# Performance work log

Hardware: AMD Instinct MI355X
Metric: run time of the kernel (lower is better)

The kernel has to match this reference:

```python
import jax, jax.numpy as jnp
import numpy as np

# SpargeAttn / spas_sage2_attn_meansim block sizes
BLKQ, BLKK = 128, 64
NUM_HEADS = 8
SIMTHRESHD1 = 0.6
CDFTHRESHD = 0.98


def _block_meta(t, blk):
    # t: [B,H,S,D] -> block means [B,H,nb,D] and min-cosine-to-mean per block [B,H,nb]
    B, H, S, D = t.shape
    nb = S // blk
    tb = t.reshape(B, H, nb, blk, D)
    m = tb.mean(axis=3)
    tn = tb / (jnp.linalg.norm(tb, axis=-1, keepdims=True) + 1e-6)
    mn = m / (jnp.linalg.norm(m, axis=-1, keepdims=True) + 1e-6)
    cos = jnp.einsum('bhnkd,bhnd->bhnk', tn, mn)
    return m, cos.min(axis=-1)


def _meansim_sparse_attention(q, k, v, scale):
    # Block-sparse attention with mean-similarity pruning (SpargeAttn meansim).
    qm, qsim = _block_meta(q, BLKQ)          # [B,H,nq,D], [B,H,nq]
    km, ksim = _block_meta(k, BLKK)          # [B,H,nk,D], [B,H,nk]
    q_self = qsim > SIMTHRESHD1              # self-similar Q blocks -> mean is representative
    k_self = ksim > SIMTHRESHD1
    # pooled attention map over block means
    pooled = jax.nn.softmax(jnp.einsum('bhqd,bhkd->bhqk', qm, km) * scale, axis=-1)
    # per Q-block row: keep highest-prob K blocks until cumulative mass >= cdfthreshd
    order = jnp.argsort(-pooled, axis=-1)
    sp = jnp.take_along_axis(pooled, order, axis=-1)
    csum = jnp.cumsum(sp, axis=-1)
    keep_sorted = (csum - sp) < CDFTHRESHD   # always keeps at least the top block
    inv = jnp.argsort(order, axis=-1)
    keep = jnp.take_along_axis(keep_sorted, inv, axis=-1)  # [B,H,nq,nk]
    # conservative fallback: non-self-similar Q/K blocks are never pruned
    block_mask = keep | (~q_self)[..., None] | (~k_self)[:, :, None, :]
    tok_mask = jnp.repeat(jnp.repeat(block_mask, BLKQ, axis=2), BLKK, axis=3)
    s = jnp.einsum('bhqd,bhkd->bhqk', q, k) * scale
    s = jnp.where(tok_mask, s, -jnp.inf)
    p = jax.nn.softmax(s, axis=-1)
    return jnp.einsum('bhqk,bhkd->bhqd', p, v)


def setup_inputs() -> dict:
    key = jax.random.key(0)
    B, L, C = 2, 2048, 512
    ks = jax.random.split(key, 3)
    x = jax.random.normal(ks[0], (B, L, C), jnp.float32)
    Wqkv = jax.random.normal(ks[1], (C, 3 * C), jnp.float32) * (C ** -0.5)
    bqkv = jnp.zeros((3 * C,), jnp.float32)
    Wproj = jax.random.normal(ks[2], (C, C), jnp.float32) * (C ** -0.5)
    bproj = jnp.zeros((C,), jnp.float32)
    return {"x": x, "Wqkv": Wqkv, "bqkv": bqkv, "Wproj": Wproj, "bproj": bproj}


def reference(x, Wqkv, bqkv, Wproj, bproj):
    B, L, C = x.shape
    H = NUM_HEADS
    D = C // H
    scale = D ** -0.5
    qkv = (x @ Wqkv + bqkv).reshape(B, L, 3, H, D)
    qkv = jnp.transpose(qkv, (2, 0, 3, 1, 4))  # [3,B,H,L,D]
    q, k, v = qkv[0], qkv[1], qkv[2]
    o = _meansim_sparse_attention(q, k, v, scale)  # [B,H,L,D]
    o = jnp.transpose(o, (0, 2, 1, 3)).reshape(B, L, C)
    return o @ Wproj + bproj
```

## Files before the change

kernel.cpp:

```cpp
#include <hip/hip_runtime.h>
#include <math.h>

typedef unsigned short ushortT;
typedef unsigned int uintT;
typedef __attribute__((ext_vector_type(8))) short short8;
typedef __attribute__((ext_vector_type(16))) float f32x16;
#define MFMA32(a, b, c) __builtin_amdgcn_mfma_f32_32x32x16_bf16((a), (b), (c), 0, 0, 0)


#define LOG2E 1.4426950408889634f

static __device__ __forceinline__ ushortT f2b(float f) {
    union { float f; uintT u; } v; v.f = f;
    uintT u = v.u;
    u += 0x7fffu + ((u >> 16) & 1u);
    return (ushortT)(u >> 16);
}
static __device__ __forceinline__ uintT pack2(float a, float b) {
    return (uintT)f2b(a) | ((uintT)f2b(b) << 16);
}
static __device__ __forceinline__ uintT pack2t(float a, float b) {
    union { float f; uintT u; } x0, x1; x0.f = a; x1.f = b;
    return __builtin_amdgcn_perm(x1.u, x0.u, 0x07060302u);
}
static __device__ __forceinline__ float blo(uintT u) {
    union { uintT u; float f; } v; v.u = u << 16; return v.f;
}
static __device__ __forceinline__ float bhi(uintT u) {
    union { uintT u; float f; } v; v.u = u & 0xffff0000u; return v.f;
}
static __device__ __forceinline__ f32x16 zero16() {
    f32x16 z;
    #pragma unroll
    for (int i = 0; i < 16; ++i) z[i] = 0.f;
    return z;
}

#define B_N 2
#define H_N 8
#define L_N 2048
#define NQB 16
#define NKB 32

__global__ __launch_bounds__(256) void prep_kernel(
    const float* __restrict__ x, ushortT* __restrict__ xb,
    const float* __restrict__ Wq, ushortT* __restrict__ Wqt,
    const float* __restrict__ Wp, ushortT* __restrict__ Wpt) {
    const int bid = blockIdx.x, t = threadIdx.x;
    __shared__ float tile[32][33];
    if (bid < 2048) {
        int i = (bid * 256 + t) * 4;
        float4 v = *(const float4*)(x + i);
        uint2 o; o.x = pack2(v.x, v.y); o.y = pack2(v.z, v.w);
        *(uint2*)(xb + i) = o;
        return;
    }
    const float* W; ushortT* Wt; int C, c0, r0;
    if (bid < 2816) {
        const int b = bid - 2048;
        W = Wq; Wt = Wqt; C = 1536;
        c0 = (b % 48) * 32; r0 = (b / 48) * 32;
    } else {
        const int b = bid - 2816;
        W = Wp; Wt = Wpt; C = 512;
        c0 = (b & 15) * 32; r0 = (b >> 4) * 32;
    }
    const int tx = t & 31, ty = t >> 5;
    #pragma unroll
    for (int i = 0; i < 4; ++i)
        tile[ty + 8 * i][tx] = W[(size_t)(r0 + ty + 8 * i) * C + c0 + tx];
    __syncthreads();
    #pragma unroll
    for (int i = 0; i < 4; ++i) {
        int rr = ty + 8 * i;
        Wt[(size_t)(c0 + rr) * 512 + r0 + tx] = f2b(tile[tx][rr]);
    }
}

__global__ __launch_bounds__(256) void qkv_gemm_kernel(
    const ushortT* __restrict__ xb, const ushortT* __restrict__ wt,
    const float* __restrict__ bias,
    ushortT* __restrict__ qb, ushortT* __restrict__ kbuf, ushortT* __restrict__ vt,
    float* __restrict__ qm, float* __restrict__ km) {
    __shared__ __align__(16) ushortT As[2][128 * 40];
    __shared__ __align__(16) ushortT Bs[2][64 * 40];
    __shared__ float sumbuf[4][64];
    const int t = threadIdx.x;
    const int l = t & 63, w = t >> 6;
    const int lm = l & 31, lh = l >> 5;
    const int rowbase = blockIdx.y * 128;
    const int colbase = blockIdx.x * 64;

    f32x16 acc[2];
    acc[0] = zero16(); acc[1] = zero16();

    const int r = t >> 1, half = t & 1;
    const ushortT* Ag = xb + (size_t)(rowbase + r) * 512 + half * 16;
    const int soA = r * 40 + half * 16;
    const int rb = t >> 2, q4 = t & 3;
    const ushortT* Bg = wt + (size_t)(colbase + rb) * 512 + q4 * 8;
    const int soB = rb * 40 + q4 * 8;

    uint4 a0, a1, b0;
    a0 = *(const uint4*)(Ag); a1 = *(const uint4*)(Ag + 8);
    b0 = *(const uint4*)(Bg);
    *(uint4*)(&As[0][soA]) = a0; *(uint4*)(&As[0][soA] + 8) = a1;
    *(uint4*)(&Bs[0][soB]) = b0;

    for (int k0 = 0; k0 < 512; k0 += 32) {
        const int cur = (k0 >> 5) & 1;
        __syncthreads();
        if (k0 < 480) {
            a0 = *(const uint4*)(Ag + k0 + 32); a1 = *(const uint4*)(Ag + k0 + 40);
            b0 = *(const uint4*)(Bg + k0 + 32);
        }
        #pragma unroll
        for (int ks = 0; ks < 2; ++ks) {
            const int ko = 16 * ks + 8 * lh;
            short8 af  = *(const short8*)(&As[cur][(32 * w + lm) * 40 + ko]);
            short8 b_0 = *(const short8*)(&Bs[cur][lm * 40 + ko]);
            short8 b_1 = *(const short8*)(&Bs[cur][(32 + lm) * 40 + ko]);
            acc[0] = MFMA32(af, b_0, acc[0]);
            acc[1] = MFMA32(af, b_1, acc[1]);
        }
        if (k0 < 480) {
            const int nxt = cur ^ 1;
            *(uint4*)(&As[nxt][soA]) = a0; *(uint4*)(&As[nxt][soA] + 8) = a1;
            *(uint4*)(&Bs[nxt][soB]) = b0;
        }
    }

    const int which = blockIdx.x >> 3;
    const int h = blockIdx.x & 7;
    const int by = blockIdx.y;
    const int b = by >> 4;
    const size_t hb = (size_t)(b * 8 + h);
    float bias2[2];
    #pragma unroll
    for (int nt = 0; nt < 2; ++nt) bias2[nt] = bias[colbase + 32 * nt + lm];
    float msum[2] = {0.f, 0.f};
    #pragma unroll
    for (int nt = 0; nt < 2; ++nt) {
        const int dd = 32 * nt + lm;
        #pragma unroll
        for (int rg = 0; rg < 16; ++rg) {
            const int row_local = 32 * w + (rg & 3) + 8 * (rg >> 2) + 4 * lh;
            const int ll = (rowbase + row_local) & 2047;
            float val = acc[nt][rg] + bias2[nt];
            if (which == 0) {
                val *= 0.125f;
                msum[nt] += val;
                qb[(hb * 2048 + ll) * 64 + dd] = f2b(val * LOG2E);
            } else if (which == 1) {
                msum[nt] += val;
                kbuf[(hb * 2048 + ll) * 64 + dd] = f2b(val);
            } else {
                vt[hb * 131072 + (size_t)(ll >> 6) * 4096 + dd * 64 + (ll & 63)] = f2b(val);
            }
        }
    }
    if (which == 2) return;
    #pragma unroll
    for (int nt = 0; nt < 2; ++nt) {
        float s = msum[nt] + __shfl_xor(msum[nt], 32);
        if (l < 32) sumbuf[w][32 * nt + lm] = s;
    }
    __syncthreads();
    if (which == 0) {
        if (t < 64) {
            const int qbi = by & 15;
            qm[(hb * 16 + qbi) * 64 + t] =
                (sumbuf[0][t] + sumbuf[1][t] + sumbuf[2][t] + sumbuf[3][t]) * (1.0f / 128.0f);
        }
    } else {
        if (t < 128) {
            const int d = t & 63, pair = t >> 6;
            const int kbi = 2 * (by & 15) + pair;
            km[(hb * 32 + kbi) * 64 + d] =
                (sumbuf[2 * pair][d] + sumbuf[2 * pair + 1][d]) * (1.0f / 64.0f);
        }
    }
}

__global__ __launch_bounds__(256) void cos_kernel(const ushortT* __restrict__ qb,
                                                  const ushortT* __restrict__ kbuf,
                                                  const float* __restrict__ qm,
                                                  const float* __restrict__ km,
                                                  float* __restrict__ qs,
                                                  float* __restrict__ ks) {
    const int bh = blockIdx.y, t = threadIdx.x;
    const int l = t & 63, w = t >> 6;
    __shared__ float mS[64];
    __shared__ float wmin[4];
    if (blockIdx.z == 0) {
        if (blockIdx.x >= 16) return;
        const int qbk = blockIdx.x;
        if (t < 64) mS[t] = qm[((size_t)bh * 16 + qbk) * 64 + t];
        __syncthreads();
        float qn = 0.f;
        #pragma unroll
        for (int d = 0; d < 64; ++d) qn += mS[d] * mS[d];
        qn = sqrtf(qn);
        const int tok = t >> 1, half = t & 1;
        const ushortT* qrow = qb + ((size_t)bh * 2048 + qbk * 128 + tok) * 64 + half * 32;
        float dot = 0.f, nn = 0.f;
        #pragma unroll
        for (int c = 0; c < 4; ++c) {
            uint4 u = *(const uint4*)(qrow + c * 8);
            const int db = half * 32 + c * 8;
            float f0 = blo(u.x), f1 = bhi(u.x), f2 = blo(u.y), f3 = bhi(u.y);
            float f4 = blo(u.z), f5 = bhi(u.z), f6 = blo(u.w), f7 = bhi(u.w);
            dot += f0 * mS[db] + f1 * mS[db + 1] + f2 * mS[db + 2] + f3 * mS[db + 3]
                 + f4 * mS[db + 4] + f5 * mS[db + 5] + f6 * mS[db + 6] + f7 * mS[db + 7];
            nn += f0 * f0 + f1 * f1 + f2 * f2 + f3 * f3 + f4 * f4 + f5 * f5 + f6 * f6 + f7 * f7;
        }
        dot += __shfl_xor(dot, 1);
        nn += __shfl_xor(nn, 1);
        float cosv = dot / ((sqrtf(nn) + 1e-6f) * (qn + 1e-6f));
        #pragma unroll
        for (int off = 1; off < 64; off <<= 1) cosv = fminf(cosv, __shfl_xor(cosv, off));
        if (l == 0) wmin[w] = cosv;
        __syncthreads();
        if (t == 0)
            qs[bh * 16 + qbk] = fminf(fminf(wmin[0], wmin[1]), fminf(wmin[2], wmin[3]));
    } else {
        const int kbk = blockIdx.x;
        if (t < 64) mS[t] = km[((size_t)bh * 32 + kbk) * 64 + t];
        __syncthreads();
        float kn = 0.f;
        #pragma unroll
        for (int d = 0; d < 64; ++d) kn += mS[d] * mS[d];
        kn = sqrtf(kn);
        const int tok = t >> 2, quarter = t & 3;
        const ushortT* krow = kbuf + ((size_t)bh * 2048 + kbk * 64 + tok) * 64 + quarter * 16;
        float dot = 0.f, nn = 0.f;
        #pragma unroll
        for (int c = 0; c < 2; ++c) {
            uint4 u = *(const uint4*)(krow + c * 8);
            const int db = quarter * 16 + c * 8;
            float f0 = blo(u.x), f1 = bhi(u.x), f2 = blo(u.y), f3 = bhi(u.y);
            float f4 = blo(u.z), f5 = bhi(u.z), f6 = blo(u.w), f7 = bhi(u.w);
            dot += f0 * mS[db] + f1 * mS[db + 1] + f2 * mS[db + 2] + f3 * mS[db + 3]
                 + f4 * mS[db + 4] + f5 * mS[db + 5] + f6 * mS[db + 6] + f7 * mS[db + 7];
            nn += f0 * f0 + f1 * f1 + f2 * f2 + f3 * f3 + f4 * f4 + f5 * f5 + f6 * f6 + f7 * f7;
        }
        dot += __shfl_xor(dot, 1); dot += __shfl_xor(dot, 2);
        nn += __shfl_xor(nn, 1); nn += __shfl_xor(nn, 2);
        float cosv = dot / ((sqrtf(nn) + 1e-6f) * (kn + 1e-6f));
        #pragma unroll
        for (int off = 1; off < 64; off <<= 1) cosv = fminf(cosv, __shfl_xor(cosv, off));
        if (l == 0) wmin[w] = cosv;
        __syncthreads();
        if (t == 0)
            ks[bh * 32 + kbk] = fminf(fminf(wmin[0], wmin[1]), fminf(wmin[2], wmin[3]));
    }
}

__global__ __launch_bounds__(512) void mask_kernel(const float* __restrict__ qm,
                                                   const float* __restrict__ km,
                                                   const float* __restrict__ qs,
                                                   const float* __restrict__ ks,
                                                   int* __restrict__ maskp) {
    const int bh = blockIdx.x, t = threadIdx.x;
    __shared__ float qmS[16 * 64];
    __shared__ float kmS[32 * 64];
    __shared__ float pooled[16 * 32];
    __shared__ float pnorm[16 * 32];
    for (int i = t; i < 1024; i += 512) qmS[i] = qm[(size_t)bh * 1024 + i];
    for (int i = t; i < 2048; i += 512) kmS[i] = km[(size_t)bh * 2048 + i];
    __syncthreads();
    {
        const int qbi = t >> 5, kbi = t & 31;
        float dot = 0.f;
        #pragma unroll
        for (int d = 0; d < 64; ++d) dot += qmS[qbi * 64 + d] * kmS[kbi * 64 + d];
        pooled[t] = dot;
    }
    __syncthreads();
    if (t < 16) {
        float mx = -1e30f;
        #pragma unroll
        for (int kb = 0; kb < NKB; ++kb) mx = fmaxf(mx, pooled[t * 32 + kb]);
        float sum = 0.f;
        #pragma unroll
        for (int kb = 0; kb < NKB; ++kb) {
            const float e = expf(pooled[t * 32 + kb] - mx);
            pnorm[t * 32 + kb] = e;
            sum += e;
        }
        const float inv = 1.0f / sum;
        #pragma unroll
        for (int kb = 0; kb < NKB; ++kb) pnorm[t * 32 + kb] *= inv;
    }
    __syncthreads();
    {
        const int row = t >> 5, kb = t & 31;
        const float pk = pnorm[row * 32 + kb];
        float before = 0.f;
        #pragma unroll
        for (int j = 0; j < NKB; ++j) {
            const float pj = pnorm[row * 32 + j];
            if (pj > pk || (pj == pk && j < kb)) before += pj;
        }
        const bool keep = before < 0.98f;
        const bool qfb = !(qs[bh * 16 + row] > 0.6f);
        const bool kfb = !(ks[bh * 32 + kb] > 0.6f);
        maskp[((size_t)bh * 16 + row) * 32 + kb] = (keep || qfb || kfb) ? 1 : 0;
    }
}

__global__ __launch_bounds__(256) void attn_kernel(
    const ushortT* __restrict__ qb, const ushortT* __restrict__ kbuf,
    const ushortT* __restrict__ vt, const int* __restrict__ maskp,
    uintT* __restrict__ pc0, uintT* __restrict__ pc1,
    uintT* __restrict__ pc2, uintT* __restrict__ pc3, float* __restrict__ lp) {
    __shared__ __align__(16) ushortT Ks[2][64 * 72];
    __shared__ __align__(16) ushortT Vs[2][64 * 72];
    __shared__ int klist[33];
    const int t = threadIdx.x;
    const int l = t & 63, w = t >> 6;
    const int lm = l & 31, lh = l >> 5;
    const int qt = blockIdx.x, bh = blockIdx.y, kc = blockIdx.z;
    const int NC = gridDim.z;

    if (w == 0) {
        const int* mrow = maskp + ((size_t)bh * 16 + qt) * 32;
        const int keep = (l < 32) ? mrow[l] : 0;
        unsigned long long bal = __ballot(keep != 0);
        if (keep) {
            const int rank = __popcll(bal & ((1ULL << l) - 1ULL));
            klist[rank] = l;
        }
        if (l == 0) klist[32] = __popcll(bal);
    }
    const ushortT* qg = qb + ((size_t)bh * 2048 + qt * 128) * 64;
    short8 qf[4];
    #pragma unroll
    for (int ksd = 0; ksd < 4; ++ksd)
        qf[ksd] = *(const short8*)(qg + (32 * w + lm) * 64 + 16 * ksd + 8 * lh);
    __syncthreads();

    const int cnt = klist[32];
    const int per = cnt / NC, rem = cnt - per * NC;
    const int n = per + (kc < rem ? 1 : 0);
    const int s = kc * per + (kc < rem ? kc : rem);

    const ushortT* kgb = kbuf + (size_t)bh * 131072;
    const ushortT* vgb = vt + (size_t)bh * 131072;
    const int cr = t >> 3, cp = (t & 7) * 8;
    const int gK0 = cr * 64 + cp, gK1 = gK0 + 2048;
    const int sK0 = cr * 72 + cp, sK1 = sK0 + 2304;

    f32x16 oacc[2];
    oacc[0] = zero16(); oacc[1] = zero16();
    float l_i = 0.f;

    uint4 ka0, ka1, va0, va1;
    if (n > 0) {
        const int kb0 = klist[s];
        const ushortT* kg = kgb + (size_t)kb0 * 4096;
        const ushortT* vg = vgb + (size_t)kb0 * 4096;
        ka0 = *(const uint4*)(kg + gK0); ka1 = *(const uint4*)(kg + gK1);
        va0 = *(const uint4*)(vg + gK0); va1 = *(const uint4*)(vg + gK1);
        *(uint4*)(&Ks[0][sK0]) = ka0; *(uint4*)(&Ks[0][sK1]) = ka1;
        *(uint4*)(&Vs[0][sK0]) = va0; *(uint4*)(&Vs[0][sK1]) = va1;
    }

    for (int i = 0; i < n; ++i) {
        const int cur = i & 1;
        __syncthreads();
        if (i + 1 < n) {
            const int kbn = klist[s + i + 1];
            const ushortT* kg = kgb + (size_t)kbn * 4096;
            const ushortT* vg = vgb + (size_t)kbn * 4096;
            ka0 = *(const uint4*)(kg + gK0); ka1 = *(const uint4*)(kg + gK1);
            va0 = *(const uint4*)(vg + gK0); va1 = *(const uint4*)(vg + gK1);
        }
        f32x16 sacc[2];
        sacc[0] = zero16(); sacc[1] = zero16();
        #pragma unroll
        for (int ksd = 0; ksd < 4; ++ksd) {
            const int ko = 16 * ksd + 8 * lh;
            short8 kf0 = *(const short8*)(&Ks[cur][lm * 72 + ko]);
            short8 kf1 = *(const short8*)(&Ks[cur][(32 + lm) * 72 + ko]);
            sacc[0] = MFMA32(kf0, qf[ksd], sacc[0]);
            sacc[1] = MFMA32(kf1, qf[ksd], sacc[1]);
        }
        float psum0 = 0.f, psum1 = 0.f;
        uintT uu[2][4][2];
        #pragma unroll
        for (int mt = 0; mt < 2; ++mt) {
            #pragma unroll
            for (int rp = 0; rp < 8; ++rp) {
                const float e0 = exp2f(sacc[mt][2 * rp]);
                const float e1 = exp2f(sacc[mt][2 * rp + 1]);
                psum0 += e0; psum1 += e1;
                uu[mt][rp >> 1][rp & 1] = pack2t(e0, e1);
            }
        }
        float psum = psum0 + psum1;
        psum += __shfl_xor(psum, 32);
        l_i += psum;
        #pragma unroll
        for (int ksk = 0; ksk < 4; ++ksk) {
            const int mt = ksk >> 1, par = ksk & 1;
            const uintT kA = lh ? uu[mt][2 * par + 1][0] : uu[mt][2 * par][0];
            const uintT kB = lh ? uu[mt][2 * par + 1][1] : uu[mt][2 * par][1];
            const uintT sA = lh ? uu[mt][2 * par][0] : uu[mt][2 * par + 1][0];
            const uintT sB = lh ? uu[mt][2 * par][1] : uu[mt][2 * par + 1][1];
            const uintT rA = (uintT)__shfl_xor((int)sA, 32);
            const uintT rB = (uintT)__shfl_xor((int)sB, 32);
            union { uintT u[4]; short8 v; } cv;
            if (lh == 0) { cv.u[0] = kA; cv.u[1] = kB; cv.u[2] = rA; cv.u[3] = rB; }
            else         { cv.u[0] = rA; cv.u[1] = rB; cv.u[2] = kA; cv.u[3] = kB; }
            const int ko = 16 * ksk + 8 * lh;
            short8 vf0 = *(const short8*)(&Vs[cur][lm * 72 + ko]);
            short8 vf1 = *(const short8*)(&Vs[cur][(32 + lm) * 72 + ko]);
            oacc[0] = MFMA32(vf0, cv.v, oacc[0]);
            oacc[1] = MFMA32(vf1, cv.v, oacc[1]);
        }
        if (i + 1 < n) {
            const int nxt = cur ^ 1;
            *(uint4*)(&Ks[nxt][sK0]) = ka0; *(uint4*)(&Ks[nxt][sK1]) = ka1;
            *(uint4*)(&Vs[nxt][sK0]) = va0; *(uint4*)(&Vs[nxt][sK1]) = va1;
        }
    }
    if (lh == 0)
        lp[kc * 32768 + ((size_t)bh * 16 + qt) * 128 + 32 * w + lm] = l_i;
    uintT pu[16];
    #pragma unroll
    for (int mt = 0; mt < 2; ++mt)
        #pragma unroll
        for (int rp = 0; rp < 8; ++rp)
            pu[mt * 8 + rp] = pack2(oacc[mt][2 * rp], oacc[mt][2 * rp + 1]);
    uintT* pcb = (kc == 0) ? pc0 : (kc == 1) ? pc1 : (kc == 2) ? pc2 : pc3;
    uintT* pdst = pcb + (((size_t)bh * 16 + qt) * 4 + w) * 1024 + l * 4;
    #pragma unroll
    for (int i4 = 0; i4 < 4; ++i4)
        *(uint4*)(pdst + i4 * 256) =
            make_uint4(pu[i4 * 4], pu[i4 * 4 + 1], pu[i4 * 4 + 2], pu[i4 * 4 + 3]);
}

__global__ __launch_bounds__(256) void reduce_kernel(
    const uintT* __restrict__ pc0, const uintT* __restrict__ pc1,
    const uintT* __restrict__ pc2, const uintT* __restrict__ pc3,
    const float* __restrict__ lp, ushortT* __restrict__ ob, int NC) {
    const int t = threadIdx.x;
    const int l = t & 63, w = t >> 6;
    const int lm = l & 31, lh = l >> 5;
    const int qt = blockIdx.x, bh = blockIdx.y;
    const size_t base = (((size_t)bh * 16 + qt) * 4 + w) * 1024 + l * 4;
    const int qrow = 32 * w + lm;
    float accL[16], accH[16];
    #pragma unroll
    for (int i = 0; i < 16; ++i) { accL[i] = 0.f; accH[i] = 0.f; }
    float lsum = 0.f;
    #pragma unroll
    for (int c = 0; c < 4; ++c) {
        if (c >= NC) break;
        const uintT* p = (c == 0) ? pc0 : (c == 1) ? pc1 : (c == 2) ? pc2 : pc3;
        #pragma unroll
        for (int i4 = 0; i4 < 4; ++i4) {
            uint4 v = *(const uint4*)(p + base + i4 * 256);
            accL[i4 * 4 + 0] += blo(v.x); accH[i4 * 4 + 0] += bhi(v.x);
            accL[i4 * 4 + 1] += blo(v.y); accH[i4 * 4 + 1] += bhi(v.y);
            accL[i4 * 4 + 2] += blo(v.z); accH[i4 * 4 + 2] += bhi(v.z);
            accL[i4 * 4 + 3] += blo(v.w); accH[i4 * 4 + 3] += bhi(v.w);
        }
        lsum += lp[c * 32768 + ((size_t)bh * 16 + qt) * 128 + qrow];
    }
    const float invl = 1.0f / lsum;
    __syncthreads();
    ushortT* orow = ob + ((size_t)bh * 2048 + qt * 128 + qrow) * 64;
    #pragma unroll
    for (int idx = 0; idx < 16; ++idx) {
        const int mt = idx >> 3, rp = idx & 7;
        const int d0 = 32 * mt + 8 * (rp >> 1) + 4 * lh + 2 * (rp & 1);
        *(uintT*)(orow + d0) = pack2(accL[idx] * invl, accH[idx] * invl);
    }
}

__global__ __launch_bounds__(256) void proj_gemm_kernel(
    const ushortT* __restrict__ ob, const ushortT* __restrict__ wpt,
    const float* __restrict__ bias, float* __restrict__ out) {
    __shared__ __align__(16) ushortT As[2][64 * 40];
    __shared__ __align__(16) ushortT Bs[2][64 * 40];
    const int t = threadIdx.x;
    const int l = t & 63, w = t >> 6;
    const int lm = l & 31, lh = l >> 5;
    const int rh = w & 1, ch = w >> 1;
    const int rowbase = blockIdx.y * 64;
    const int colbase = blockIdx.x * 64;

    f32x16 acc = zero16();

    const int r = t >> 2, q4 = t & 3;
    const int token = rowbase + r;
    const int b2 = token >> 11, lt = token & 2047;
    const int so = r * 40 + q4 * 8;
    const ushortT* obbase = ob + ((size_t)(b2 * 8) * 2048 + lt) * 64 + q4 * 8;
    const ushortT* Bg = wpt + (size_t)(colbase + r) * 512 + q4 * 8;

    uint4 a0, b0;
    a0 = *(const uint4*)(obbase);
    b0 = *(const uint4*)(Bg);
    *(uint4*)(&As[0][so]) = a0;
    *(uint4*)(&Bs[0][so]) = b0;

    for (int k0 = 0; k0 < 512; k0 += 32) {
        const int cur = (k0 >> 5) & 1;
        __syncthreads();
        if (k0 < 480) {
            const int kn = k0 + 32;
            const ushortT* Ag = obbase + (size_t)(kn >> 6) * 131072 + (kn & 63);
            a0 = *(const uint4*)(Ag);
            b0 = *(const uint4*)(Bg + kn);
        }
        #pragma unroll
        for (int ks = 0; ks < 2; ++ks) {
            const int ko = 16 * ks + 8 * lh;
            short8 af = *(const short8*)(&As[cur][(32 * rh + lm) * 40 + ko]);
            short8 bf = *(const short8*)(&Bs[cur][(32 * ch + lm) * 40 + ko]);
            acc = MFMA32(af, bf, acc);
        }
        if (k0 < 480) {
            const int nxt = cur ^ 1;
            *(uint4*)(&As[nxt][so]) = a0;
            *(uint4*)(&Bs[nxt][so]) = b0;
        }
    }
    const int c = colbase + 32 * ch + lm;
    const float bb = bias[c];
    #pragma unroll
    for (int rg = 0; rg < 16; ++rg) {
        const int row_local = 32 * rh + (rg & 3) + 8 * (rg >> 2) + 4 * lh;
        out[(size_t)(rowbase + row_local) * 512 + c] = acc[rg] + bb;
    }
}

extern "C" void kernel_launch(void* const* d_in, const int* in_sizes, int n_in,
                              void* d_out, int out_size, void* d_ws, size_t ws_size,
                              hipStream_t stream) {
    const float* x     = (const float*)d_in[0];
    const float* Wqkv  = (const float*)d_in[1];
    const float* bqkv  = (const float*)d_in[2];
    const float* Wproj = (const float*)d_in[3];
    const float* bproj = (const float*)d_in[4];
    float* out = (float*)d_out;

    char* w = (char*)d_ws;
    ushortT* xb     = (ushortT*)(w);
    ushortT* wqkvt  = (ushortT*)(w + 4194304);
    ushortT* wprojt = (ushortT*)(w + 5767168);
    ushortT* qb     = (ushortT*)(w + 6291456);
    ushortT* kbuf   = (ushortT*)(w + 10485760);
    ushortT* vt     = (ushortT*)(w + 14680064);
    ushortT* ob     = (ushortT*)(w + 18874368);
    float*   qm     = (float*)(w + 23068672);
    float*   km     = (float*)(w + 23134208);
    float*   qs     = (float*)(w + 23265280);
    float*   ks     = (float*)(w + 23266304);
    int*     maskp  = (int*)(w + 23268352);
    float*   lp2    = (float*)(w + 23301120);
    uintT*   pc2    = (uintT*)(w + 23563264);
    uintT*   pc3    = (uintT*)(w + 27757568);
    float*   lp4    = (float*)(w + 31951872);
    const int NC = (ws_size >= 32476160) ? 4 : 2;
    float* lpA = (NC == 4) ? lp4 : lp2;

    uintT* pc0 = (uintT*)xb;
    uintT* pc1 = (uintT*)ob;
    if (NC == 2) { pc2 = pc0; pc3 = pc0; }

    prep_kernel<<<3072, 256, 0, stream>>>(x, xb, Wqkv, wqkvt, Wproj, wprojt);
    qkv_gemm_kernel<<<dim3(24, 32), 256, 0, stream>>>(xb, wqkvt, bqkv, qb, kbuf, vt, qm, km);
    cos_kernel<<<dim3(32, 16, 2), 256, 0, stream>>>(qb, kbuf, qm, km, qs, ks);
    mask_kernel<<<16, 512, 0, stream>>>(qm, km, qs, ks, maskp);
    attn_kernel<<<dim3(16, 16, NC), 256, 0, stream>>>(qb, kbuf, vt, maskp, pc0, pc1, pc2, pc3, lpA);
    reduce_kernel<<<dim3(16, 16), 256, 0, stream>>>(pc0, pc1, pc2, pc3, lpA, ob, NC);
    proj_gemm_kernel<<<dim3(8, 64), 256, 0, stream>>>(ob, wprojt, bproj, out);
}
```

Before: 154.0 us.

## Fuse cosine-sim into mask kernel and fold split-K reduce into attention

Merges the per-block min-cosine computation into the mask kernel so Q/K self-similarity flags stay in shared memory, and removes the separate reduce kernel by having the last-finishing attention split (tracked with an atomic counter zeroed in prep) combine the partial outputs. This removes two kernel launches and global round-trips of intermediate stats. In exchange the cosine work now runs on only 16 blocks with serial per-thread row loops, and the atomic/threadfence tail adds serialization; workspace layout and split-count selection also change.

```diff
diff --git a/kernel.cpp b/kernel.cpp
--- a/kernel.cpp
+++ b/kernel.cpp
@@ -45,10 +45,12 @@
 __global__ __launch_bounds__(256) void prep_kernel(
     const float* __restrict__ x, ushortT* __restrict__ xb,
     const float* __restrict__ Wq, ushortT* __restrict__ Wqt,
-    const float* __restrict__ Wp, ushortT* __restrict__ Wpt) {
+    const float* __restrict__ Wp, ushortT* __restrict__ Wpt,
+    int* __restrict__ cnt) {
     const int bid = blockIdx.x, t = threadIdx.x;
     __shared__ float tile[32][33];
     if (bid < 2048) {
+        if (bid == 0) cnt[t] = 0;
         int i = (bid * 256 + t) * 4;
         float4 v = *(const float4*)(x + i);
         uint2 o; o.x = pack2(v.x, v.y); o.y = pack2(v.z, v.w);
@@ -182,93 +184,33 @@
     }
 }
 
-__global__ __launch_bounds__(256) void cos_kernel(const ushortT* __restrict__ qb,
-                                                  const ushortT* __restrict__ kbuf,
-                                                  const float* __restrict__ qm,
-                                                  const float* __restrict__ km,
-                                                  float* __restrict__ qs,
-                                                  float* __restrict__ ks) {
-    const int bh = blockIdx.y, t = threadIdx.x;
-    const int l = t & 63, w = t >> 6;
-    __shared__ float mS[64];
-    __shared__ float wmin[4];
-    if (blockIdx.z == 0) {
-        if (blockIdx.x >= 16) return;
-        const int qbk = blockIdx.x;
-        if (t < 64) mS[t] = qm[((size_t)bh * 16 + qbk) * 64 + t];
-        __syncthreads();
-        float qn = 0.f;
-        #pragma unroll
-        for (int d = 0; d < 64; ++d) qn += mS[d] * mS[d];
-        qn = sqrtf(qn);
-        const int tok = t >> 1, half = t & 1;
-        const ushortT* qrow = qb + ((size_t)bh * 2048 + qbk * 128 + tok) * 64 + half * 32;
-        float dot = 0.f, nn = 0.f;
-        #pragma unroll
-        for (int c = 0; c < 4; ++c) {
-            uint4 u = *(const uint4*)(qrow + c * 8);
-            const int db = half * 32 + c * 8;
-            float f0 = blo(u.x), f1 = bhi(u.x), f2 = blo(u.y), f3 = bhi(u.y);
-            float f4 = blo(u.z), f5 = bhi(u.z), f6 = blo(u.w), f7 = bhi(u.w);
-            dot += f0 * mS[db] + f1 * mS[db + 1] + f2 * mS[db + 2] + f3 * mS[db + 3]
-                 + f4 * mS[db + 4] + f5 * mS[db + 5] + f6 * mS[db + 6] + f7 * mS[db + 7];
-            nn += f0 * f0 + f1 * f1 + f2 * f2 + f3 * f3 + f4 * f4 + f5 * f5 + f6 * f6 + f7 * f7;
-        }
-        dot += __shfl_xor(dot, 1);
-        nn += __shfl_xor(nn, 1);
-        float cosv = dot / ((sqrtf(nn) + 1e-6f) * (qn + 1e-6f));
-        #pragma unroll
-        for (int off = 1; off < 64; off <<= 1) cosv = fminf(cosv, __shfl_xor(cosv, off));
-        if (l == 0) wmin[w] = cosv;
-        __syncthreads();
-        if (t == 0)
-            qs[bh * 16 + qbk] = fminf(fminf(wmin[0], wmin[1]), fminf(wmin[2], wmin[3]));
-    } else {
-        const int kbk = blockIdx.x;
-        if (t < 64) mS[t] = km[((size_t)bh * 32 + kbk) * 64 + t];
-        __syncthreads();
-        float kn = 0.f;
-        #pragma unroll
-        for (int d = 0; d < 64; ++d) kn += mS[d] * mS[d];
-        kn = sqrtf(kn);
-        const int tok = t >> 2, quarter = t & 3;
-        const ushortT* krow = kbuf + ((size_t)bh * 2048 + kbk * 64 + tok) * 64 + quarter * 16;
-        float dot = 0.f, nn = 0.f;
-        #pragma unroll
-        for (int c = 0; c < 2; ++c) {
-            uint4 u = *(const uint4*)(krow + c * 8);
-            const int db = quarter * 16 + c * 8;
-            float f0 = blo(u.x), f1 = bhi(u.x), f2 = blo(u.y), f3 = bhi(u.y);
-            float f4 = blo(u.z), f5 = bhi(u.z), f6 = blo(u.w), f7 = bhi(u.w);
-            dot += f0 * mS[db] + f1 * mS[db + 1] + f2 * mS[db + 2] + f3 * mS[db + 3]
-                 + f4 * mS[db + 4] + f5 * mS[db + 5] + f6 * mS[db + 6] + f7 * mS[db + 7];
-            nn += f0 * f0 + f1 * f1 + f2 * f2 + f3 * f3 + f4 * f4 + f5 * f5 + f6 * f6 + f7 * f7;
-        }
-        dot += __shfl_xor(dot, 1); dot += __shfl_xor(dot, 2);
-        nn += __shfl_xor(nn, 1); nn += __shfl_xor(nn, 2);
-        float cosv = dot / ((sqrtf(nn) + 1e-6f) * (kn + 1e-6f));
-        #pragma unroll
-        for (int off = 1; off < 64; off <<= 1) cosv = fminf(cosv, __shfl_xor(cosv, off));
-        if (l == 0) wmin[w] = cosv;
-        __syncthreads();
-        if (t == 0)
-            ks[bh * 32 + kbk] = fminf(fminf(wmin[0], wmin[1]), fminf(wmin[2], wmin[3]));
-    }
-}
-
-__global__ __launch_bounds__(512) void mask_kernel(const float* __restrict__ qm,
-                                                   const float* __restrict__ km,
-                                                   const float* __restrict__ qs,
-                                                   const float* __restrict__ ks,
-                                                   int* __restrict__ maskp) {
+__global__ __launch_bounds__(512) void cosmask_kernel(
+    const ushortT* __restrict__ qb, const ushortT* __restrict__ kbuf,
+    const float* __restrict__ qm, const float* __restrict__ km,
+    int* __restrict__ maskp) {
     const int bh = blockIdx.x, t = threadIdx.x;
-    __shared__ float qmS[16 * 64];
-    __shared__ float kmS[32 * 64];
-    __shared__ float pooled[16 * 32];
-    __shared__ float pnorm[16 * 32];
+    __shared__ float qmS[1024];
+    __shared__ float kmS[2048];
+    __shared__ float nrm[48];
+    __shared__ float pooled[512];
+    __shared__ float pnorm[512];
+    __shared__ float tokcos[2048];
+    __shared__ float qsS[16], ksS[32];
     for (int i = t; i < 1024; i += 512) qmS[i] = qm[(size_t)bh * 1024 + i];
     for (int i = t; i < 2048; i += 512) kmS[i] = km[(size_t)bh * 2048 + i];
     __syncthreads();
+    if (t < 16) {
+        float s = 0.f;
+        #pragma unroll
+        for (int d = 0; d < 64; ++d) s += qmS[t * 64 + d] * qmS[t * 64 + d];
+        nrm[t] = sqrtf(s);
+    } else if (t < 48) {
+        const int kb = t - 16;
+        float s = 0.f;
+        #pragma unroll
+        for (int d = 0; d < 64; ++d) s += kmS[kb * 64 + d] * kmS[kb * 64 + d];
+        nrm[16 + kb] = sqrtf(s);
+    }
     {
         const int qbi = t >> 5, kbi = t & 31;
         float dot = 0.f;
@@ -277,20 +219,67 @@
         pooled[t] = dot;
     }
     __syncthreads();
+    for (int tok = t; tok < 2048; tok += 512) {
+        const int qbk = tok >> 7;
+        const ushortT* row = qb + ((size_t)bh * 2048 + tok) * 64;
+        const float* m = &qmS[qbk * 64];
+        float dot = 0.f, nn = 0.f;
+        #pragma unroll
+        for (int c = 0; c < 8; ++c) {
+            uint4 u = *(const uint4*)(row + c * 8);
+            float f0 = blo(u.x), f1 = bhi(u.x), f2 = blo(u.y), f3 = bhi(u.y);
+            float f4 = blo(u.z), f5 = bhi(u.z), f6 = blo(u.w), f7 = bhi(u.w);
+            const int db = c * 8;
+            dot += f0 * m[db] + f1 * m[db + 1] + f2 * m[db + 2] + f3 * m[db + 3]
+                 + f4 * m[db + 4] + f5 * m[db + 5] + f6 * m[db + 6] + f7 * m[db + 7];
+            nn += f0 * f0 + f1 * f1 + f2 * f2 + f3 * f3 + f4 * f4 + f5 * f5 + f6 * f6 + f7 * f7;
+        }
+        tokcos[tok] = dot / ((sqrtf(nn) + 1e-6f) * (nrm[qbk] + 1e-6f));
+    }
+    __syncthreads();
     if (t < 16) {
+        float mn = 1e30f;
+        for (int i = 0; i < 128; ++i) mn = fminf(mn, tokcos[t * 128 + i]);
+        qsS[t] = mn;
+    }
+    __syncthreads();
+    for (int tok = t; tok < 2048; tok += 512) {
+        const int kbk = tok >> 6;
+        const ushortT* row = kbuf + ((size_t)bh * 2048 + tok) * 64;
+        const float* m = &kmS[kbk * 64];
+        float dot = 0.f, nn = 0.f;
+        #pragma unroll
+        for (int c = 0; c < 8; ++c) {
+            uint4 u = *(const uint4*)(row + c * 8);
+            float f0 = blo(u.x), f1 = bhi(u.x), f2 = blo(u.y), f3 = bhi(u.y);
+            float f4 = blo(u.z), f5 = bhi(u.z), f6 = blo(u.w), f7 = bhi(u.w);
+            const int db = c * 8;
+            dot += f0 * m[db] + f1 * m[db + 1] + f2 * m[db + 2] + f3 * m[db + 3]
+                 + f4 * m[db + 4] + f5 * m[db + 5] + f6 * m[db + 6] + f7 * m[db + 7];
+            nn += f0 * f0 + f1 * f1 + f2 * f2 + f3 * f3 + f4 * f4 + f5 * f5 + f6 * f6 + f7 * f7;
+        }
+        tokcos[tok] = dot / ((sqrtf(nn) + 1e-6f) * (nrm[16 + kbk] + 1e-6f));
+    }
+    __syncthreads();
+    if (t < 32) {
+        float mn = 1e30f;
+        for (int i = 0; i < 64; ++i) mn = fminf(mn, tokcos[t * 64 + i]);
+        ksS[t] = mn;
+    } else if (t >= 64 && t < 80) {
+        const int row = t - 64;
         float mx = -1e30f;
         #pragma unroll
-        for (int kb = 0; kb < NKB; ++kb) mx = fmaxf(mx, pooled[t * 32 + kb]);
+        for (int kb = 0; kb < NKB; ++kb) mx = fmaxf(mx, pooled[row * 32 + kb]);
         float sum = 0.f;
         #pragma unroll
         for (int kb = 0; kb < NKB; ++kb) {
-            const float e = expf(pooled[t * 32 + kb] - mx);
-            pnorm[t * 32 + kb] = e;
+            const float e = expf(pooled[row * 32 + kb] - mx);
+            pnorm[row * 32 + kb] = e;
             sum += e;
         }
         const float inv = 1.0f / sum;
         #pragma unroll
-        for (int kb = 0; kb < NKB; ++kb) pnorm[t * 32 + kb] *= inv;
+        for (int kb = 0; kb < NKB; ++kb) pnorm[row * 32 + kb] *= inv;
     }
     __syncthreads();
     {
@@ -303,8 +292,8 @@
             if (pj > pk || (pj == pk && j < kb)) before += pj;
         }
         const bool keep = before < 0.98f;
-        const bool qfb = !(qs[bh * 16 + row] > 0.6f);
-        const bool kfb = !(ks[bh * 32 + kb] > 0.6f);
+        const bool qfb = !(qsS[row] > 0.6f);
+        const bool kfb = !(ksS[kb] > 0.6f);
         maskp[((size_t)bh * 16 + row) * 32 + kb] = (keep || qfb || kfb) ? 1 : 0;
     }
 }
@@ -313,10 +302,12 @@
     const ushortT* __restrict__ qb, const ushortT* __restrict__ kbuf,
     const ushortT* __restrict__ vt, const int* __restrict__ maskp,
     uintT* __restrict__ pc0, uintT* __restrict__ pc1,
-    uintT* __restrict__ pc2, uintT* __restrict__ pc3, float* __restrict__ lp) {
+    uintT* __restrict__ pc2, uintT* __restrict__ pc3,
+    float* __restrict__ lp, int* cnt, ushortT* ob) {
     __shared__ __align__(16) ushortT Ks[2][64 * 72];
     __shared__ __align__(16) ushortT Vs[2][64 * 72];
     __shared__ int klist[33];
+    __shared__ int lastf;
     const int t = threadIdx.x;
     const int l = t & 63, w = t >> 6;
     const int lm = l & 31, lh = l >> 5;
@@ -340,8 +331,8 @@
         qf[ksd] = *(const short8*)(qg + (32 * w + lm) * 64 + 16 * ksd + 8 * lh);
     __syncthreads();
 
-    const int cnt = klist[32];
-    const int per = cnt / NC, rem = cnt - per * NC;
+    const int cnt_k = klist[32];
+    const int per = cnt_k / NC, rem = cnt_k - per * NC;
     const int n = per + (kc < rem ? 1 : 0);
     const int s = kc * per + (kc < rem ? kc : rem);
 
@@ -434,26 +425,24 @@
         for (int rp = 0; rp < 8; ++rp)
             pu[mt * 8 + rp] = pack2(oacc[mt][2 * rp], oacc[mt][2 * rp + 1]);
     uintT* pcb = (kc == 0) ? pc0 : (kc == 1) ? pc1 : (kc == 2) ? pc2 : pc3;
-    uintT* pdst = pcb + (((size_t)bh * 16 + qt) * 4 + w) * 1024 + l * 4;
+    const size_t base = (((size_t)bh * 16 + qt) * 4 + w) * 1024 + l * 4;
     #pragma unroll
     for (int i4 = 0; i4 < 4; ++i4)
-        *(uint4*)(pdst + i4 * 256) =
+        *(uint4*)(pcb + base + i4 * 256) =
             make_uint4(pu[i4 * 4], pu[i4 * 4 + 1], pu[i4 * 4 + 2], pu[i4 * 4 + 3]);
-}
-
-__global__ __launch_bounds__(256) void reduce_kernel(
-    const uintT* __restrict__ pc0, const uintT* __restrict__ pc1,
-    const uintT* __restrict__ pc2, const uintT* __restrict__ pc3,
-    const float* __restrict__ lp, ushortT* __restrict__ ob, int NC) {
-    const int t = threadIdx.x;
-    const int l = t & 63, w = t >> 6;
-    const int lm = l & 31, lh = l >> 5;
-    const int qt = blockIdx.x, bh = blockIdx.y;
-    const size_t base = (((size_t)bh * 16 + qt) * 4 + w) * 1024 + l * 4;
+
+    __threadfence();
+    if (t == 0) {
+        const int prev = atomicAdd(cnt + (bh * 16 + qt), 1);
+        lastf = (prev == NC - 1) ? 1 : 0;
+    }
+    __syncthreads();
+    if (!lastf) return;
+    __threadfence();
+    float accL[16], accH[16];
+    #pragma unroll
+    for (int i = 0; i < 16; ++i) { accL[i] = 0.f; accH[i] = 0.f; }
     const int qrow = 32 * w + lm;
-    float accL[16], accH[16];
-    #pragma unroll
-    for (int i = 0; i < 16; ++i) { accL[i] = 0.f; accH[i] = 0.f; }
     float lsum = 0.f;
     #pragma unroll
     for (int c = 0; c < 4; ++c) {
@@ -470,7 +459,6 @@
         lsum += lp[c * 32768 + ((size_t)bh * 16 + qt) * 128 + qrow];
     }
     const float invl = 1.0f / lsum;
-    __syncthreads();
     ushortT* orow = ob + ((size_t)bh * 2048 + qt * 128 + qrow) * 64;
     #pragma unroll
     for (int idx = 0; idx < 16; ++idx) {
@@ -558,25 +546,23 @@
     ushortT* ob     = (ushortT*)(w + 18874368);
     float*   qm     = (float*)(w + 23068672);
     float*   km     = (float*)(w + 23134208);
-    float*   qs     = (float*)(w + 23265280);
-    float*   ks     = (float*)(w + 23266304);
-    int*     maskp  = (int*)(w + 23268352);
-    float*   lp2    = (float*)(w + 23301120);
-    uintT*   pc2    = (uintT*)(w + 23563264);
-    uintT*   pc3    = (uintT*)(w + 27757568);
-    float*   lp4    = (float*)(w + 31951872);
-    const int NC = (ws_size >= 32476160) ? 4 : 2;
-    float* lpA = (NC == 4) ? lp4 : lp2;
-
-    uintT* pc0 = (uintT*)xb;
-    uintT* pc1 = (uintT*)ob;
-    if (NC == 2) { pc2 = pc0; pc3 = pc0; }
-
-    prep_kernel<<<3072, 256, 0, stream>>>(x, xb, Wqkv, wqkvt, Wproj, wprojt);
+    int*     maskp  = (int*)(w + 23265280);
+    int*     cnt    = (int*)(w + 23298048);
+    float*   lp     = (float*)(w + 23299072);
+    uintT*   pc1    = (uintT*)(w + 23823360);
+    uintT*   pc2    = (uintT*)(w + 28017664);
+    uintT*   pc3    = (uintT*)(w + 32211968);
+    uintT*   pc0    = (uintT*)xb;
+
+    const int NC = (ws_size >= 36406272 + 4096) ? 4
+                 : (ws_size >= 28017664 + 4194304) ? 2 : 1;
+    if (NC < 4) { pc2 = pc0; pc3 = pc0; }
+    if (NC < 2) { pc1 = pc0; }
+
+    prep_kernel<<<3072, 256, 0, stream>>>(x, xb, Wqkv, wqkvt, Wproj, wprojt, cnt);
     qkv_gemm_kernel<<<dim3(24, 32), 256, 0, stream>>>(xb, wqkvt, bqkv, qb, kbuf, vt, qm, km);
-    cos_kernel<<<dim3(32, 16, 2), 256, 0, stream>>>(qb, kbuf, qm, km, qs, ks);
-    mask_kernel<<<16, 512, 0, stream>>>(qm, km, qs, ks, maskp);
-    attn_kernel<<<dim3(16, 16, NC), 256, 0, stream>>>(qb, kbuf, vt, maskp, pc0, pc1, pc2, pc3, lpA);
-    reduce_kernel<<<dim3(16, 16), 256, 0, stream>>>(pc0, pc1, pc2, pc3, lpA, ob, NC);
+    cosmask_kernel<<<16, 512, 0, stream>>>(qb, kbuf, qm, km, maskp);
+    attn_kernel<<<dim3(16, 16, NC), 256, 0, stream>>>(qb, kbuf, vt, maskp,
+                                                      pc0, pc1, pc2, pc3, lp, cnt, ob);
     proj_gemm_kernel<<<dim3(8, 64), 256, 0, stream>>>(ob, wprojt, bproj, out);
 }
```

Measured after the change: 292.3 us. 1.9x slower.
